# Performance work log

Measured on AMD Instinct MI355X. Metric: run time of the kernel, lower is better.

Reference implementation:

```python
import jax, jax.numpy as jnp
import numpy as np

BINS = 6
THRESH = 0.2
OUT_HW = (240, 240)


def _normalize(x, lo=0.0, hi=1.0):
    # torch: if max-min==0 return zeros, else affine rescale to [lo, hi]
    mn, mx = x.min(), x.max()
    rng = mx - mn
    safe = jnp.where(rng == 0, 1.0, rng)
    out = (x - mn) / safe * (hi - lo) + lo
    return jnp.where(rng == 0, jnp.zeros_like(x), out)


def _ponder(x):
    w = (x.max() - x.mean()) ** 2
    return _normalize(x) * w


def _zero_border(x):
    # zero first/last row and column (works batched over leading dims)
    return (x.at[..., 0, :].set(0.0)
             .at[..., :, 0].set(0.0)
             .at[..., -1, :].set(0.0)
             .at[..., :, -1].set(0.0))


def _rarity(ch):
    # ch: [H, W] single feature channel
    ch = _zero_border(ch)
    ch = _normalize(ch, 0.0, 256.0)
    # torch.histc(bins=BINS, min=0, max=256): last bin includes the max value
    bin_idx = jnp.clip(jnp.floor(ch / (256.0 / BINS)), 0, BINS - 1).astype(jnp.int32)
    hist = jnp.zeros((BINS,), ch.dtype).at[bin_idx].add(1.0)
    hist = -jnp.log(hist / hist.sum() + 0.0001)
    # (channel * bins - 1).long().clamp(0, bins-1): .long() truncates toward zero
    gidx = jnp.clip(jnp.trunc(ch * BINS - 1.0), 0, BINS - 1).astype(jnp.int32)
    dst = _normalize(hist[gidx], 0.0, 1.0)
    return _ponder(dst)


def _apply_rarity(layer):
    # layer: [1, C, H, W] -> per-channel rarity, ponderated sum, threshold
    ch = layer[0]  # [C, H, W]
    r = jax.vmap(_rarity)(ch)  # [C, H, W]
    rz = _zero_border(r)
    # channel 0 keeps its border (torch code only zeroes borders for i >= 1)
    maps = jnp.concatenate([r[:1], rz[1:]], axis=0)
    proc = jax.vmap(_ponder)(maps).sum(0)
    proc = _normalize(proc, 0.0, 1.0)
    return jnp.where(proc < THRESH, 0.0, proc)


def _group(layer):
    resized = jax.image.resize(_apply_rarity(layer), OUT_HW, 'bilinear')
    # pack of one layer: fuse_itti == map_ponderation of the single map
    return _normalize(_ponder(resized), 0.0, 256.0)


def _forward(l1, l2, l3, l4, l5):
    groups = jnp.stack([_group(l) for l in (l1, l2, l3, l4, l5)], axis=-1)  # [240,240,5]
    return groups.sum(-1), groups


def setup_inputs() -> dict:
    key = jax.random.key(0)
    ks = jax.random.split(key, 5)
    shapes = [(1, 64, 480, 480), (1, 128, 240, 240), (1, 256, 120, 120),
              (1, 512, 60, 60), (1, 512, 30, 30)]
    return {f"l{i+1}": jax.random.uniform(ks[i], shapes[i], jnp.float32)
            for i in range(5)}


def reference(l1, l2, l3, l4, l5):
    return _forward(l1, l2, l3, l4, l5)
```

## Files before the change

### kernel.cpp

```cpp
#include <hip/hip_runtime.h>
#include <math.h>

#define TPB 256

constexpr int DIMS_[5]  = {480, 240, 120, 60, 30};
constexpr int CHS_ [5]  = {64, 128, 256, 512, 512};
constexpr int CHB_ [5]  = {0, 64, 192, 448, 960};
constexpr int TOTCH     = 1472;
constexpr int PROCB_[5] = {0, 230400, 288000, 302400, 306000};
constexpr int PROCTOT   = 306900;

constexpr int O_CHMIN = 0;
constexpr int O_CHMAX = 1472;
constexpr int O_HIST  = 2944;
constexpr int O_GCNT  = 11776;
constexpr int O_CLUT  = 20608;
constexpr int O_BSUM  = O_CLUT + 16 * 1472;
constexpr int O_PMIN  = O_BSUM + 5;
constexpr int O_PMAX  = O_PMIN + 5;
constexpr int O_S3MIN = O_PMAX + 5;
constexpr int O_S3MAX = O_S3MIN + 5;
constexpr int O_S3SUM = O_S3MAX + 5;
constexpr int O_PROC  = 44192;
constexpr int O_RESZ  = O_PROC + PROCTOT;

struct P {
  const float* in[5];
  float* ws;
};

__global__ void k_init(float* ws) {
  int i = blockIdx.x * TPB + threadIdx.x;
  if (i >= O_PROC) return;
  unsigned v = 0u;
  if (i < O_CHMAX) v = 0x7F800000u;
  else if (i >= O_PMIN  && i < O_PMAX)  v = 0x7F800000u;
  else if (i >= O_S3MIN && i < O_S3MAX) v = 0x7F800000u;
  ((unsigned*)ws)[i] = v;
}

template <int L>
__device__ void bodyA(int local, const float* __restrict__ in, float* ws) {
  constexpr int D = DIMS_[L], HW = D * D, HW4 = HW / 4;
  constexpr int BPC = (HW4 + 4095) / 4096;
  int ch = local / BPC, chunk = local % BPC;
  int nvec = HW4 - chunk * 4096; if (nvec > 4096) nvec = 4096;
  const float4* pv = (const float4*)(in + (size_t)ch * HW) + (size_t)chunk * 4096;
  int t = threadIdx.x;
  float mn = INFINITY, mx = 0.0f;
  for (int i = 0; i < 16; i++) {
    int vi = i * TPB + t;
    if (vi < nvec) {
      float4 v = pv[vi];
      float vv[4] = {v.x, v.y, v.z, v.w};
      int e0 = (chunk * 4096 + vi) * 4;
      #pragma unroll
      for (int j = 0; j < 4; j++) {
        int e = e0 + j, y = e / D, x = e - y * D;
        bool inr = ((unsigned)(x - 1) < (unsigned)(D - 2)) && ((unsigned)(y - 1) < (unsigned)(D - 2));
        float s = inr ? vv[j] : 0.0f;
        mn = fminf(mn, s); mx = fmaxf(mx, s);
      }
    }
  }
  for (int o = 32; o; o >>= 1) { mn = fminf(mn, __shfl_down(mn, o)); mx = fmaxf(mx, __shfl_down(mx, o)); }
  __shared__ float smn[4], smx[4];
  int w = t >> 6;
  if ((t & 63) == 0) { smn[w] = mn; smx[w] = mx; }
  __syncthreads();
  if (t == 0) {
    mn = fminf(fminf(smn[0], smn[1]), fminf(smn[2], smn[3]));
    mx = fmaxf(fmaxf(smx[0], smx[1]), fmaxf(smx[2], smx[3]));
    int g = CHB_[L] + ch;
    atomicMin((unsigned*)ws + O_CHMIN + g, __float_as_uint(mn));
    atomicMax((unsigned*)ws + O_CHMAX + g, __float_as_uint(mx));
  }
}
__global__ void kA(P p) {
  int b = blockIdx.x;
  if      (b <  960) bodyA<0>(b,        p.in[0], p.ws);
  else if (b < 1472) bodyA<1>(b -  960, p.in[1], p.ws);
  else if (b < 1728) bodyA<2>(b - 1472, p.in[2], p.ws);
  else if (b < 2240) bodyA<3>(b - 1728, p.in[3], p.ws);
  else               bodyA<4>(b - 2240, p.in[4], p.ws);
}

__global__ void kTB(P p) {
  int ch = blockIdx.x;
  float* ws = p.ws;
  int l = (ch < 64) ? 0 : (ch < 192) ? 1 : (ch < 448) ? 2 : (ch < 960) ? 3 : 4;
  int D = DIMS_[l];
  float mn = ws[O_CHMIN + ch], mx = ws[O_CHMAX + ch];
  float rng = mx - mn;
  float th0, th1, th2, th3, th4, tg0, tg1, tg2, tg3, tg4;
  if (rng == 0.0f) {
    th0 = th1 = th2 = th3 = th4 = tg0 = tg1 = tg2 = tg3 = tg4 = INFINITY;
  } else {
    th0 = mn + rng * (1.0f / 6.0f); th1 = mn + rng * (2.0f / 6.0f);
    th2 = mn + rng * (3.0f / 6.0f); th3 = mn + rng * (4.0f / 6.0f);
    th4 = mn + rng * (5.0f / 6.0f);
    tg0 = mn + rng * (2.0f / 1536.0f); tg1 = mn + rng * (3.0f / 1536.0f);
    tg2 = mn + rng * (4.0f / 1536.0f); tg3 = mn + rng * (5.0f / 1536.0f);
    tg4 = mn + rng * (6.0f / 1536.0f);
  }
  int t = threadIdx.x;
  if (t == 0) {
    float* T = ws + O_CLUT + (size_t)ch * 16;
    T[0] = th0; T[1] = th1; T[2] = th2; T[3] = th3; T[4] = th4;
    T[5] = tg0; T[6] = tg1; T[7] = tg2; T[8] = tg3; T[9] = tg4;
  }
  const float* in = p.in[l] + (size_t)(ch - CHB_[l]) * D * D;
  int nb = 4 * D - 4;
  unsigned cH0 = 0, cH1 = 0, cH2 = 0, cH3 = 0, cH4 = 0;
  unsigned cG0 = 0, cG1 = 0, cG2 = 0, cG3 = 0, cG4 = 0, nval = 0;
  for (int j = t; j < nb; j += TPB) {
    int y, x;
    if (j < D)            { y = 0;               x = j;          }
    else if (j < 2 * D)   { y = D - 1;           x = j - D;      }
    else if (j < 3 * D - 2){ y = j - 2 * D + 1;  x = 0;          }
    else                  { y = j - (3 * D - 2) + 1; x = D - 1;  }
    float v = in[y * D + x];
    nval += __popcll(__ballot(1));
    cH0 += __popcll(__ballot(v >= th0)); cH1 += __popcll(__ballot(v >= th1));
    cH2 += __popcll(__ballot(v >= th2)); cH3 += __popcll(__ballot(v >= th3));
    cH4 += __popcll(__ballot(v >= th4));
    cG0 += __popcll(__ballot(v >= tg0)); cG1 += __popcll(__ballot(v >= tg1));
    cG2 += __popcll(__ballot(v >= tg2)); cG3 += __popcll(__ballot(v >= tg3));
    cG4 += __popcll(__ballot(v >= tg4));
  }
  unsigned* H = (unsigned*)ws + O_HIST + ch * 6;
  unsigned* G = (unsigned*)ws + O_GCNT + ch * 6;
  if ((t & 63) == 0) {
    atomicAdd(H + 0, (unsigned)(-(int)(nval - cH0)));
    atomicAdd(H + 1, (unsigned)(-(int)(cH0 - cH1)));
    atomicAdd(H + 2, (unsigned)(-(int)(cH1 - cH2)));
    atomicAdd(H + 3, (unsigned)(-(int)(cH2 - cH3)));
    atomicAdd(H + 4, (unsigned)(-(int)(cH3 - cH4)));
    atomicAdd(H + 5, (unsigned)(-(int)cH4));
    atomicAdd(G + 0, (unsigned)(-(int)(nval - cG0)));
    atomicAdd(G + 1, (unsigned)(-(int)(cG0 - cG1)));
    atomicAdd(G + 2, (unsigned)(-(int)(cG1 - cG2)));
    atomicAdd(G + 3, (unsigned)(-(int)(cG2 - cG3)));
    atomicAdd(G + 4, (unsigned)(-(int)(cG3 - cG4)));
    atomicAdd(G + 5, (unsigned)(-(int)cG4));
  }
  if (t == 0) {
    int hb0 = (0.0f >= th0) + (0.0f >= th1) + (0.0f >= th2) + (0.0f >= th3) + (0.0f >= th4);
    int gb0 = (0.0f >= tg0) + (0.0f >= tg1) + (0.0f >= tg2) + (0.0f >= tg3) + (0.0f >= tg4);
    atomicAdd(H + hb0, (unsigned)nb);
    atomicAdd(G + gb0, (unsigned)nb);
  }
}

template <int L>
__device__ void bodyB(int local, const float* __restrict__ in, float* ws) {
  constexpr int D = DIMS_[L], HW = D * D, HW4 = HW / 4;
  constexpr int BPC = (HW4 + 4095) / 4096;
  int ch = local / BPC, chunk = local % BPC;
  int g = CHB_[L] + ch;
  const float* T = ws + O_CLUT + (size_t)g * 16;
  float th0 = T[0], th1 = T[1], th2 = T[2], th3 = T[3], th4 = T[4];
  float tg0 = T[5], tg1 = T[6], tg2 = T[7], tg3 = T[8], tg4 = T[9];
  int nvec = HW4 - chunk * 4096; if (nvec > 4096) nvec = 4096;
  const float4* pv = (const float4*)(in + (size_t)ch * HW) + (size_t)chunk * 4096;
  int t = threadIdx.x;
  unsigned cH0 = 0, cH1 = 0, cH2 = 0, cH3 = 0, cH4 = 0;
  unsigned cG0 = 0, cG1 = 0, cG2 = 0, cG3 = 0, cG4 = 0, nv4 = 0;
  for (int i = 0; i < 16; i++) {
    int vi = i * TPB + t;
    if (vi < nvec) {
      float4 v = pv[vi];
      nv4 += __popcll(__ballot(1));
      float vv[4] = {v.x, v.y, v.z, v.w};
      #pragma unroll
      for (int j = 0; j < 4; j++) {
        float x = vv[j];
        cH0 += __popcll(__ballot(x >= th0)); cH1 += __popcll(__ballot(x >= th1));
        cH2 += __popcll(__ballot(x >= th2)); cH3 += __popcll(__ballot(x >= th3));
        cH4 += __popcll(__ballot(x >= th4));
        cG0 += __popcll(__ballot(x >= tg0)); cG1 += __popcll(__ballot(x >= tg1));
        cG2 += __popcll(__ballot(x >= tg2)); cG3 += __popcll(__ballot(x >= tg3));
        cG4 += __popcll(__ballot(x >= tg4));
      }
    }
  }
  if ((t & 63) == 0) {
    unsigned tot = nv4 * 4u;
    unsigned* H = (unsigned*)ws + O_HIST + g * 6;
    unsigned* G = (unsigned*)ws + O_GCNT + g * 6;
    atomicAdd(H + 0, tot - cH0); atomicAdd(H + 1, cH0 - cH1);
    atomicAdd(H + 2, cH1 - cH2); atomicAdd(H + 3, cH2 - cH3);
    atomicAdd(H + 4, cH3 - cH4); atomicAdd(H + 5, cH4);
    atomicAdd(G + 0, tot - cG0); atomicAdd(G + 1, cG0 - cG1);
    atomicAdd(G + 2, cG1 - cG2); atomicAdd(G + 3, cG2 - cG3);
    atomicAdd(G + 4, cG3 - cG4); atomicAdd(G + 5, cG4);
  }
}
__global__ void kB(P p) {
  int b = blockIdx.x;
  if      (b <  960) bodyB<0>(b,        p.in[0], p.ws);
  else if (b < 1472) bodyB<1>(b -  960, p.in[1], p.ws);
  else if (b < 1728) bodyB<2>(b - 1472, p.in[2], p.ws);
  else if (b < 2240) bodyB<3>(b - 1728, p.in[3], p.ws);
  else               bodyB<4>(b - 2240, p.in[4], p.ws);
}

__global__ void kS(P p) {
  int ch = blockIdx.x * TPB + threadIdx.x;
  if (ch >= TOTCH) return;
  float* ws = p.ws;
  int l = (ch < 64) ? 0 : (ch < 192) ? 1 : (ch < 448) ? 2 : (ch < 960) ? 3 : 4;
  int D = DIMS_[l];
  int HW = D * D;
  int c0 = ch - CHB_[l];
  unsigned hc[6], gc[6];
  unsigned* H = (unsigned*)ws + O_HIST + ch * 6;
  unsigned* G = (unsigned*)ws + O_GCNT + ch * 6;
  #pragma unroll
  for (int k = 0; k < 6; k++) { hc[k] = H[k]; gc[k] = G[k]; }
  float HWf = (float)HW;
  float nh[6];
  #pragma unroll
  for (int k = 0; k < 6; k++) nh[k] = -logf((float)hc[k] / HWf + 1e-4f);
  float dmn = INFINITY, dmx = -INFINITY;
  #pragma unroll
  for (int k = 0; k < 6; k++) if (gc[k]) { dmn = fminf(dmn, nh[k]); dmx = fmaxf(dmx, nh[k]); }
  float dr = dmx - dmn;
  float dstn[6];
  #pragma unroll
  for (int k = 0; k < 6; k++) dstn[k] = (dr == 0.0f) ? 0.0f : ((nh[k] - dmn) / dr);
  float maxv = (dr == 0.0f) ? 0.0f : 1.0f;
  double s1 = 0.0;
  #pragma unroll
  for (int k = 0; k < 6; k++) s1 += (double)gc[k] * (double)dstn[k];
  float mean1 = (float)(s1 / (double)HW);
  float w1 = maxv - mean1; w1 *= w1;
  float lut1[6];
  #pragma unroll
  for (int k = 0; k < 6; k++) lut1[k] = dstn[k] * w1;
  const float* T = ws + O_CLUT + (size_t)ch * 16;
  int gb = (0.0f >= T[5]) + (0.0f >= T[6]) + (0.0f >= T[7]) + (0.0f >= T[8]) + (0.0f >= T[9]);
  unsigned bcnt = (unsigned)(4 * D - 4);
  float lmn, lmx;
  double s2 = 0.0;
  if (c0 == 0) {
    lmn = INFINITY; lmx = -INFINITY;
    #pragma unroll
    for (int k = 0; k < 6; k++) if (gc[k]) {
      lmn = fminf(lmn, lut1[k]); lmx = fmaxf(lmx, lut1[k]);
      s2 += (double)gc[k] * (double)lut1[k];
    }
  } else {
    lmn = 0.0f; lmx = 0.0f;
    #pragma unroll
    for (int k = 0; k < 6; k++) {
      unsigned ic = gc[k] - ((k == gb) ? bcnt : 0u);
      if (ic) {
        lmn = fminf(lmn, lut1[k]); lmx = fmaxf(lmx, lut1[k]);
        s2 += (double)ic * (double)lut1[k];
      }
    }
  }
  float mean2 = (float)(s2 / (double)HW);
  float w2 = lmx - mean2; w2 *= w2;
  float r2 = lmx - lmn;
  float lout[6];
  #pragma unroll
  for (int k = 0; k < 6; k++) lout[k] = (r2 == 0.0f) ? 0.0f : (((lut1[k] - lmn) / r2) * w2);
  float* LT = ws + O_CLUT + (size_t)ch * 16 + 10;
  #pragma unroll
  for (int k = 0; k < 6; k++) LT[k] = lout[k];
  float bc = (c0 == 0) ? lout[gb] : ((r2 == 0.0f) ? 0.0f : (((0.0f - lmn) / r2) * w2));
  atomicAdd(ws + O_BSUM + l, bc);
}

template <int L>
__device__ void bodyC(int local, const float* __restrict__ in, float* ws,
                      float* slut, float* sred) {
  constexpr int D = DIMS_[L], HW = D * D, HW4 = HW / 4, C = CHS_[L];
  constexpr int Q = C / 4;
  int t = threadIdx.x, lane = t & 63, w = t >> 6;
  const float* gl = ws + O_CLUT + (size_t)CHB_[L] * 16;
  for (int i = t; i < C * 16; i += TPB) slut[i] = gl[i];
  __syncthreads();
  int p4 = local * 64 + lane;
  bool valid = p4 < HW4;
  float a0 = 0.0f, a1 = 0.0f, a2 = 0.0f, a3 = 0.0f;
  if (valid) {
    const float4* bp = (const float4*)in + p4 + (size_t)(w * Q) * HW4;
    const float* su = slut + (size_t)(w * Q) * 16;
    #pragma unroll 4
    for (int c = 0; c < Q; c++) {
      float4 v = bp[(size_t)c * HW4];
      const float* cl = su + c * 16 + 5;
      float g0 = cl[0], g1 = cl[1], g2 = cl[2], g3 = cl[3], g4 = cl[4];
      float l0 = cl[5], l1 = cl[6], l2 = cl[7], l3 = cl[8], l4 = cl[9], l5 = cl[10];
      float s;
      s = (v.x >= g0) ? l1 : l0; s = (v.x >= g1) ? l2 : s; s = (v.x >= g2) ? l3 : s;
      s = (v.x >= g3) ? l4 : s;  s = (v.x >= g4) ? l5 : s; a0 += s;
      s = (v.y >= g0) ? l1 : l0; s = (v.y >= g1) ? l2 : s; s = (v.y >= g2) ? l3 : s;
      s = (v.y >= g3) ? l4 : s;  s = (v.y >= g4) ? l5 : s; a1 += s;
      s = (v.z >= g0) ? l1 : l0; s = (v.z >= g1) ? l2 : s; s = (v.z >= g2) ? l3 : s;
      s = (v.z >= g3) ? l4 : s;  s = (v.z >= g4) ? l5 : s; a2 += s;
      s = (v.w >= g0) ? l1 : l0; s = (v.w >= g1) ? l2 : s; s = (v.w >= g2) ? l3 : s;
      s = (v.w >= g3) ? l4 : s;  s = (v.w >= g4) ? l5 : s; a3 += s;
    }
  }
  sred[0 * 256 + w * 64 + lane] = a0;
  sred[1 * 256 + w * 64 + lane] = a1;
  sred[2 * 256 + w * 64 + lane] = a2;
  sred[3 * 256 + w * 64 + lane] = a3;
  __syncthreads();
  if (w == 0) {
    float o[4];
    #pragma unroll
    for (int j = 0; j < 4; j++)
      o[j] = sred[j * 256 + lane] + sred[j * 256 + 64 + lane] +
             sred[j * 256 + 128 + lane] + sred[j * 256 + 192 + lane];
    float bs = ws[O_BSUM + L];
    int px0 = p4 * 4;
    #pragma unroll
    for (int j = 0; j < 4; j++) {
      int px = px0 + j, y = px / D, x = px - y * D;
      bool inr = ((unsigned)(x - 1) < (unsigned)(D - 2)) && ((unsigned)(y - 1) < (unsigned)(D - 2));
      if (!inr) o[j] = bs;
    }
    float mn, mx;
    if (valid) {
      float4* procL4 = (float4*)(ws + O_PROC + PROCB_[L]);
      procL4[p4] = make_float4(o[0], o[1], o[2], o[3]);
      mn = fminf(fminf(o[0], o[1]), fminf(o[2], o[3]));
      mx = fmaxf(fmaxf(o[0], o[1]), fmaxf(o[2], o[3]));
    } else { mn = INFINITY; mx = 0.0f; }
    for (int s = 32; s; s >>= 1) { mn = fminf(mn, __shfl_down(mn, s)); mx = fmaxf(mx, __shfl_down(mx, s)); }
    if (lane == 0) {
      atomicMin((unsigned*)ws + O_PMIN + L, __float_as_uint(mn));
      atomicMax((unsigned*)ws + O_PMAX + L, __float_as_uint(mx));
    }
  }
}
__global__ __launch_bounds__(TPB) void kC(P p) {
  __shared__ float slut[512 * 16];
  __shared__ float sred[1024];
  int b = blockIdx.x;
  if      (b <  900) bodyC<0>(b,        p.in[0], p.ws, slut, sred);
  else if (b < 1125) bodyC<1>(b -  900, p.in[1], p.ws, slut, sred);
  else if (b < 1182) bodyC<2>(b - 1125, p.in[2], p.ws, slut, sred);
  else if (b < 1197) bodyC<3>(b - 1182, p.in[3], p.ws, slut, sred);
  else               bodyC<4>(b - 1197, p.in[4], p.ws, slut, sred);
}

template <int L>
__device__ float bodyF(int px, float* ws) {
  constexpr int D = DIMS_[L];
  constexpr float INV = (float)D / 240.0f;
  constexpr float KS = (INV > 1.0f) ? INV : 1.0f;
  int oy = px / 240, ox = px - oy * 240;
  float mnv = __uint_as_float(((unsigned*)ws)[O_PMIN + L]);
  float mxv = __uint_as_float(((unsigned*)ws)[O_PMAX + L]);
  float pr = mxv - mnv;
  const float* procL = ws + O_PROC + PROCB_[L];
  float sfy = ((float)oy + 0.5f) * INV - 0.5f;
  float sfx = ((float)ox + 0.5f) * INV - 0.5f;
  int y0 = (int)ceilf(sfy - KS);  if (y0 < 0) y0 = 0;
  int y1 = (int)floorf(sfy + KS); if (y1 > D - 1) y1 = D - 1;
  int x0 = (int)ceilf(sfx - KS);  if (x0 < 0) x0 = 0;
  int x1 = (int)floorf(sfx + KS); if (x1 > D - 1) x1 = D - 1;
  float wsx = 0.0f;
  for (int jx = x0; jx <= x1; jx++) wsx += fmaxf(1.0f - fabsf(sfx - (float)jx) / KS, 0.0f);
  float acc = 0.0f, wsy = 0.0f;
  for (int jy = y0; jy <= y1; jy++) {
    float wy = fmaxf(1.0f - fabsf(sfy - (float)jy) / KS, 0.0f);
    wsy += wy;
    if (wy > 0.0f) {
      const float* row = procL + jy * D;
      float rs = 0.0f;
      for (int jx = x0; jx <= x1; jx++) {
        float wx = fmaxf(1.0f - fabsf(sfx - (float)jx) / KS, 0.0f);
        if (wx > 0.0f) {
          float v = row[jx];
          float tv = (pr == 0.0f) ? 0.0f : ((v - mnv) / pr);
          tv = (tv < 0.2f) ? 0.0f : tv;
          rs += wx * tv;
        }
      }
      acc += wy * rs;
    }
  }
  return acc / (wsy * wsx);
}
__global__ void kF(P p) {
  float* ws = p.ws;
  int b = blockIdx.x, l = b / 225;
  int px = (b - l * 225) * TPB + threadIdx.x;
  float res;
  switch (l) {
    case 0: res = bodyF<0>(px, ws); break;
    case 1: res = bodyF<1>(px, ws); break;
    case 2: res = bodyF<2>(px, ws); break;
    case 3: res = bodyF<3>(px, ws); break;
    default: res = bodyF<4>(px, ws); break;
  }
  ws[O_RESZ + l * 57600 + px] = res;
  float mn = res, mx = res, s = res;
  for (int o = 32; o; o >>= 1) {
    mn = fminf(mn, __shfl_down(mn, o));
    mx = fmaxf(mx, __shfl_down(mx, o));
    s += __shfl_down(s, o);
  }
  __shared__ float smn[4], smx[4], ssm[4];
  int t = threadIdx.x, w = t >> 6;
  if ((t & 63) == 0) { smn[w] = mn; smx[w] = mx; ssm[w] = s; }
  __syncthreads();
  if (t == 0) {
    mn = fminf(fminf(smn[0], smn[1]), fminf(smn[2], smn[3]));
    mx = fmaxf(fmaxf(smx[0], smx[1]), fmaxf(smx[2], smx[3]));
    s = ssm[0] + ssm[1] + ssm[2] + ssm[3];
    atomicMin((unsigned*)ws + O_S3MIN + l, __float_as_uint(mn));
    atomicMax((unsigned*)ws + O_S3MAX + l, __float_as_uint(mx));
    atomicAdd(ws + O_S3SUM + l, s);
  }
}

__global__ void kG2(P p, float* __restrict__ out) {
  float* ws = p.ws;
  int px = blockIdx.x * TPB + threadIdx.x;
  float sum = 0.0f;
  #pragma unroll
  for (int l = 0; l < 5; l++) {
    float v = ws[O_RESZ + l * 57600 + px];
    float mn3 = __uint_as_float(((unsigned*)ws)[O_S3MIN + l]);
    float mx3 = __uint_as_float(((unsigned*)ws)[O_S3MAX + l]);
    float mean3 = ws[O_S3SUM + l] / 57600.0f;
    float r3 = mx3 - mn3;
    float ov;
    if (r3 == 0.0f) ov = 0.0f;
    else {
      float w3 = mx3 - mean3; w3 *= w3;
      if (w3 == 0.0f) ov = 0.0f;
      else ov = ((v - mn3) / r3) * w3 / w3 * 256.0f;
    }
    out[57600 + px * 5 + l] = ov;
    sum += ov;
  }
  out[px] = sum;
}

extern "C" void kernel_launch(void* const* d_in, const int* in_sizes, int n_in,
                              void* d_out, int out_size, void* d_ws, size_t ws_size,
                              hipStream_t stream) {
  (void)in_sizes; (void)n_in; (void)out_size; (void)ws_size;
  P p;
  for (int i = 0; i < 5; i++) p.in[i] = (const float*)d_in[i];
  p.ws = (float*)d_ws;
  float* out = (float*)d_out;

  k_init<<<(O_PROC + TPB - 1) / TPB, TPB, 0, stream>>>(p.ws);
  kA  <<<2752, TPB, 0, stream>>>(p);
  kTB <<<1472, TPB, 0, stream>>>(p);
  kB  <<<2752, TPB, 0, stream>>>(p);
  kS  <<<6,    TPB, 0, stream>>>(p);
  kC  <<<1201, TPB, 0, stream>>>(p);
  kF  <<<1125, TPB, 0, stream>>>(p);
  kG2 <<<225,  TPB, 0, stream>>>(p, out);
}
```

Baseline: 339.3 us.

## Split channel loop in kC across 64-channel chunks, drop border kernel

Result: faster. 294.0 us (-13.4%).

```diff
diff --git a/kernel.cpp b/kernel.cpp
--- a/kernel.cpp
+++ b/kernel.cpp
@@ -23,15 +23,29 @@
 constexpr int O_S3SUM = O_S3MAX + 5;
 constexpr int O_PROC  = 44192;
 constexpr int O_RESZ  = O_PROC + PROCTOT;
+constexpr int N_INIT  = O_PROC + PROCTOT;
 
 struct P {
   const float* in[5];
   float* ws;
 };
 
+__device__ __forceinline__ void mk_hthr(float mn, float rng, float* th) {
+  if (rng == 0.0f) { th[0]=th[1]=th[2]=th[3]=th[4]=INFINITY; return; }
+  th[0] = mn + rng * (1.0f / 6.0f); th[1] = mn + rng * (2.0f / 6.0f);
+  th[2] = mn + rng * (3.0f / 6.0f); th[3] = mn + rng * (4.0f / 6.0f);
+  th[4] = mn + rng * (5.0f / 6.0f);
+}
+__device__ __forceinline__ void mk_gthr(float mn, float rng, float* tg) {
+  if (rng == 0.0f) { tg[0]=tg[1]=tg[2]=tg[3]=tg[4]=INFINITY; return; }
+  tg[0] = mn + rng * (2.0f / 1536.0f); tg[1] = mn + rng * (3.0f / 1536.0f);
+  tg[2] = mn + rng * (4.0f / 1536.0f); tg[3] = mn + rng * (5.0f / 1536.0f);
+  tg[4] = mn + rng * (6.0f / 1536.0f);
+}
+
 __global__ void k_init(float* ws) {
   int i = blockIdx.x * TPB + threadIdx.x;
-  if (i >= O_PROC) return;
+  if (i >= N_INIT) return;
   unsigned v = 0u;
   if (i < O_CHMAX) v = 0x7F800000u;
   else if (i >= O_PMIN  && i < O_PMAX)  v = 0x7F800000u;
@@ -85,82 +99,17 @@
   else               bodyA<4>(b - 2240, p.in[4], p.ws);
 }
 
-__global__ void kTB(P p) {
-  int ch = blockIdx.x;
-  float* ws = p.ws;
-  int l = (ch < 64) ? 0 : (ch < 192) ? 1 : (ch < 448) ? 2 : (ch < 960) ? 3 : 4;
-  int D = DIMS_[l];
-  float mn = ws[O_CHMIN + ch], mx = ws[O_CHMAX + ch];
-  float rng = mx - mn;
-  float th0, th1, th2, th3, th4, tg0, tg1, tg2, tg3, tg4;
-  if (rng == 0.0f) {
-    th0 = th1 = th2 = th3 = th4 = tg0 = tg1 = tg2 = tg3 = tg4 = INFINITY;
-  } else {
-    th0 = mn + rng * (1.0f / 6.0f); th1 = mn + rng * (2.0f / 6.0f);
-    th2 = mn + rng * (3.0f / 6.0f); th3 = mn + rng * (4.0f / 6.0f);
-    th4 = mn + rng * (5.0f / 6.0f);
-    tg0 = mn + rng * (2.0f / 1536.0f); tg1 = mn + rng * (3.0f / 1536.0f);
-    tg2 = mn + rng * (4.0f / 1536.0f); tg3 = mn + rng * (5.0f / 1536.0f);
-    tg4 = mn + rng * (6.0f / 1536.0f);
-  }
-  int t = threadIdx.x;
-  if (t == 0) {
-    float* T = ws + O_CLUT + (size_t)ch * 16;
-    T[0] = th0; T[1] = th1; T[2] = th2; T[3] = th3; T[4] = th4;
-    T[5] = tg0; T[6] = tg1; T[7] = tg2; T[8] = tg3; T[9] = tg4;
-  }
-  const float* in = p.in[l] + (size_t)(ch - CHB_[l]) * D * D;
-  int nb = 4 * D - 4;
-  unsigned cH0 = 0, cH1 = 0, cH2 = 0, cH3 = 0, cH4 = 0;
-  unsigned cG0 = 0, cG1 = 0, cG2 = 0, cG3 = 0, cG4 = 0, nval = 0;
-  for (int j = t; j < nb; j += TPB) {
-    int y, x;
-    if (j < D)            { y = 0;               x = j;          }
-    else if (j < 2 * D)   { y = D - 1;           x = j - D;      }
-    else if (j < 3 * D - 2){ y = j - 2 * D + 1;  x = 0;          }
-    else                  { y = j - (3 * D - 2) + 1; x = D - 1;  }
-    float v = in[y * D + x];
-    nval += __popcll(__ballot(1));
-    cH0 += __popcll(__ballot(v >= th0)); cH1 += __popcll(__ballot(v >= th1));
-    cH2 += __popcll(__ballot(v >= th2)); cH3 += __popcll(__ballot(v >= th3));
-    cH4 += __popcll(__ballot(v >= th4));
-    cG0 += __popcll(__ballot(v >= tg0)); cG1 += __popcll(__ballot(v >= tg1));
-    cG2 += __popcll(__ballot(v >= tg2)); cG3 += __popcll(__ballot(v >= tg3));
-    cG4 += __popcll(__ballot(v >= tg4));
-  }
-  unsigned* H = (unsigned*)ws + O_HIST + ch * 6;
-  unsigned* G = (unsigned*)ws + O_GCNT + ch * 6;
-  if ((t & 63) == 0) {
-    atomicAdd(H + 0, (unsigned)(-(int)(nval - cH0)));
-    atomicAdd(H + 1, (unsigned)(-(int)(cH0 - cH1)));
-    atomicAdd(H + 2, (unsigned)(-(int)(cH1 - cH2)));
-    atomicAdd(H + 3, (unsigned)(-(int)(cH2 - cH3)));
-    atomicAdd(H + 4, (unsigned)(-(int)(cH3 - cH4)));
-    atomicAdd(H + 5, (unsigned)(-(int)cH4));
-    atomicAdd(G + 0, (unsigned)(-(int)(nval - cG0)));
-    atomicAdd(G + 1, (unsigned)(-(int)(cG0 - cG1)));
-    atomicAdd(G + 2, (unsigned)(-(int)(cG1 - cG2)));
-    atomicAdd(G + 3, (unsigned)(-(int)(cG2 - cG3)));
-    atomicAdd(G + 4, (unsigned)(-(int)(cG3 - cG4)));
-    atomicAdd(G + 5, (unsigned)(-(int)cG4));
-  }
-  if (t == 0) {
-    int hb0 = (0.0f >= th0) + (0.0f >= th1) + (0.0f >= th2) + (0.0f >= th3) + (0.0f >= th4);
-    int gb0 = (0.0f >= tg0) + (0.0f >= tg1) + (0.0f >= tg2) + (0.0f >= tg3) + (0.0f >= tg4);
-    atomicAdd(H + hb0, (unsigned)nb);
-    atomicAdd(G + gb0, (unsigned)nb);
-  }
-}
-
 template <int L>
 __device__ void bodyB(int local, const float* __restrict__ in, float* ws) {
   constexpr int D = DIMS_[L], HW = D * D, HW4 = HW / 4;
   constexpr int BPC = (HW4 + 4095) / 4096;
+  constexpr int DQ = D / 4;
   int ch = local / BPC, chunk = local % BPC;
   int g = CHB_[L] + ch;
-  const float* T = ws + O_CLUT + (size_t)g * 16;
-  float th0 = T[0], th1 = T[1], th2 = T[2], th3 = T[3], th4 = T[4];
-  float tg0 = T[5], tg1 = T[6], tg2 = T[7], tg3 = T[8], tg4 = T[9];
+  float mn = ws[O_CHMIN + g], mx = ws[O_CHMAX + g], rng = mx - mn;
+  float th[5], tg[5];
+  mk_hthr(mn, rng, th);
+  mk_gthr(mn, rng, tg);
   int nvec = HW4 - chunk * 4096; if (nvec > 4096) nvec = 4096;
   const float4* pv = (const float4*)(in + (size_t)ch * HW) + (size_t)chunk * 4096;
   int t = threadIdx.x;
@@ -170,17 +119,34 @@
     int vi = i * TPB + t;
     if (vi < nvec) {
       float4 v = pv[vi];
+      float vv[4] = {v.x, v.y, v.z, v.w};
+      int f4i = chunk * 4096 + vi;
+      if constexpr (D % 4 == 0) {
+        int y = f4i / DQ, xq = f4i - y * DQ;
+        if (y == 0 || y == D - 1) { vv[0] = vv[1] = vv[2] = vv[3] = 0.0f; }
+        else {
+          if (xq == 0)      vv[0] = 0.0f;
+          if (xq == DQ - 1) vv[3] = 0.0f;
+        }
+      } else {
+        int e0 = f4i * 4;
+        #pragma unroll
+        for (int j = 0; j < 4; j++) {
+          int e = e0 + j, y = e / D, x = e - y * D;
+          bool inr = ((unsigned)(x - 1) < (unsigned)(D - 2)) && ((unsigned)(y - 1) < (unsigned)(D - 2));
+          if (!inr) vv[j] = 0.0f;
+        }
+      }
       nv4 += __popcll(__ballot(1));
-      float vv[4] = {v.x, v.y, v.z, v.w};
       #pragma unroll
       for (int j = 0; j < 4; j++) {
         float x = vv[j];
-        cH0 += __popcll(__ballot(x >= th0)); cH1 += __popcll(__ballot(x >= th1));
-        cH2 += __popcll(__ballot(x >= th2)); cH3 += __popcll(__ballot(x >= th3));
-        cH4 += __popcll(__ballot(x >= th4));
-        cG0 += __popcll(__ballot(x >= tg0)); cG1 += __popcll(__ballot(x >= tg1));
-        cG2 += __popcll(__ballot(x >= tg2)); cG3 += __popcll(__ballot(x >= tg3));
-        cG4 += __popcll(__ballot(x >= tg4));
+        cH0 += __popcll(__ballot(x >= th[0])); cH1 += __popcll(__ballot(x >= th[1]));
+        cH2 += __popcll(__ballot(x >= th[2])); cH3 += __popcll(__ballot(x >= th[3]));
+        cH4 += __popcll(__ballot(x >= th[4]));
+        cG0 += __popcll(__ballot(x >= tg[0])); cG1 += __popcll(__ballot(x >= tg[1]));
+        cG2 += __popcll(__ballot(x >= tg[2])); cG3 += __popcll(__ballot(x >= tg[3]));
+        cG4 += __popcll(__ballot(x >= tg[4]));
       }
     }
   }
@@ -238,8 +204,10 @@
   float lut1[6];
   #pragma unroll
   for (int k = 0; k < 6; k++) lut1[k] = dstn[k] * w1;
-  const float* T = ws + O_CLUT + (size_t)ch * 16;
-  int gb = (0.0f >= T[5]) + (0.0f >= T[6]) + (0.0f >= T[7]) + (0.0f >= T[8]) + (0.0f >= T[9]);
+  float mnc = ws[O_CHMIN + ch], mxc = ws[O_CHMAX + ch];
+  float tg[5];
+  mk_gthr(mnc, mxc - mnc, tg);
+  int gb = (0.0f >= tg[0]) + (0.0f >= tg[1]) + (0.0f >= tg[2]) + (0.0f >= tg[3]) + (0.0f >= tg[4]);
   unsigned bcnt = (unsigned)(4 * D - 4);
   float lmn, lmx;
   double s2 = 0.0;
@@ -267,9 +235,11 @@
   float lout[6];
   #pragma unroll
   for (int k = 0; k < 6; k++) lout[k] = (r2 == 0.0f) ? 0.0f : (((lut1[k] - lmn) / r2) * w2);
-  float* LT = ws + O_CLUT + (size_t)ch * 16 + 10;
-  #pragma unroll
-  for (int k = 0; k < 6; k++) LT[k] = lout[k];
+  float* T = ws + O_CLUT + (size_t)ch * 16;
+  #pragma unroll
+  for (int k = 0; k < 5; k++) T[5 + k] = tg[k];
+  #pragma unroll
+  for (int k = 0; k < 6; k++) T[10 + k] = lout[k];
   float bc = (c0 == 0) ? lout[gb] : ((r2 == 0.0f) ? 0.0f : (((0.0f - lmn) / r2) * w2));
   atomicAdd(ws + O_BSUM + l, bc);
 }
@@ -278,19 +248,22 @@
 __device__ void bodyC(int local, const float* __restrict__ in, float* ws,
                       float* slut, float* sred) {
   constexpr int D = DIMS_[L], HW = D * D, HW4 = HW / 4, C = CHS_[L];
-  constexpr int Q = C / 4;
+  constexpr int NT  = (HW4 + 63) / 64;
+  constexpr int NCH = C / 64;
+  int tile = local % NT, chunk = local / NT;
+  int cbase = CHB_[L] + chunk * 64;
   int t = threadIdx.x, lane = t & 63, w = t >> 6;
-  const float* gl = ws + O_CLUT + (size_t)CHB_[L] * 16;
-  for (int i = t; i < C * 16; i += TPB) slut[i] = gl[i];
+  const float* gl = ws + O_CLUT + (size_t)cbase * 16;
+  for (int i = t; i < 1024; i += TPB) slut[i] = gl[i];
   __syncthreads();
-  int p4 = local * 64 + lane;
+  int p4 = tile * 64 + lane;
   bool valid = p4 < HW4;
   float a0 = 0.0f, a1 = 0.0f, a2 = 0.0f, a3 = 0.0f;
   if (valid) {
-    const float4* bp = (const float4*)in + p4 + (size_t)(w * Q) * HW4;
-    const float* su = slut + (size_t)(w * Q) * 16;
+    const float4* bp = (const float4*)in + (size_t)(chunk * 64 + w * 16) * HW4 + p4;
+    const float* su = slut + (w * 16) * 16;
     #pragma unroll 4
-    for (int c = 0; c < Q; c++) {
+    for (int c = 0; c < 16; c++) {
       float4 v = bp[(size_t)c * HW4];
       const float* cl = su + c * 16 + 5;
       float g0 = cl[0], g1 = cl[1], g2 = cl[2], g3 = cl[3], g4 = cl[4];
@@ -311,43 +284,75 @@
   sred[2 * 256 + w * 64 + lane] = a2;
   sred[3 * 256 + w * 64 + lane] = a3;
   __syncthreads();
-  if (w == 0) {
+  if (w == 0 && valid) {
     float o[4];
     #pragma unroll
     for (int j = 0; j < 4; j++)
       o[j] = sred[j * 256 + lane] + sred[j * 256 + 64 + lane] +
              sred[j * 256 + 128 + lane] + sred[j * 256 + 192 + lane];
     float bs = ws[O_BSUM + L];
+    float* procL = ws + O_PROC + PROCB_[L];
     int px0 = p4 * 4;
-    #pragma unroll
-    for (int j = 0; j < 4; j++) {
-      int px = px0 + j, y = px / D, x = px - y * D;
-      bool inr = ((unsigned)(x - 1) < (unsigned)(D - 2)) && ((unsigned)(y - 1) < (unsigned)(D - 2));
-      if (!inr) o[j] = bs;
-    }
-    float mn, mx;
-    if (valid) {
-      float4* procL4 = (float4*)(ws + O_PROC + PROCB_[L]);
-      procL4[p4] = make_float4(o[0], o[1], o[2], o[3]);
-      mn = fminf(fminf(o[0], o[1]), fminf(o[2], o[3]));
-      mx = fmaxf(fmaxf(o[0], o[1]), fmaxf(o[2], o[3]));
-    } else { mn = INFINITY; mx = 0.0f; }
-    for (int s = 32; s; s >>= 1) { mn = fminf(mn, __shfl_down(mn, s)); mx = fmaxf(mx, __shfl_down(mx, s)); }
-    if (lane == 0) {
-      atomicMin((unsigned*)ws + O_PMIN + L, __float_as_uint(mn));
-      atomicMax((unsigned*)ws + O_PMAX + L, __float_as_uint(mx));
+    if constexpr (NCH == 1) {
+      #pragma unroll
+      for (int j = 0; j < 4; j++) {
+        int px = px0 + j, y = px / D, x = px - y * D;
+        bool inr = ((unsigned)(x - 1) < (unsigned)(D - 2)) && ((unsigned)(y - 1) < (unsigned)(D - 2));
+        if (!inr) o[j] = bs;
+      }
+      ((float4*)procL)[p4] = make_float4(o[0], o[1], o[2], o[3]);
+    } else {
+      #pragma unroll
+      for (int j = 0; j < 4; j++) {
+        int px = px0 + j, y = px / D, x = px - y * D;
+        bool inr = ((unsigned)(x - 1) < (unsigned)(D - 2)) && ((unsigned)(y - 1) < (unsigned)(D - 2));
+        if (inr) atomicAdd(procL + px, o[j]);
+        else if (chunk == 0) procL[px] = bs;
+      }
     }
   }
 }
 __global__ __launch_bounds__(TPB) void kC(P p) {
-  __shared__ float slut[512 * 16];
+  __shared__ float slut[1024];
   __shared__ float sred[1024];
   int b = blockIdx.x;
   if      (b <  900) bodyC<0>(b,        p.in[0], p.ws, slut, sred);
-  else if (b < 1125) bodyC<1>(b -  900, p.in[1], p.ws, slut, sred);
-  else if (b < 1182) bodyC<2>(b - 1125, p.in[2], p.ws, slut, sred);
-  else if (b < 1197) bodyC<3>(b - 1182, p.in[3], p.ws, slut, sred);
-  else               bodyC<4>(b - 1197, p.in[4], p.ws, slut, sred);
+  else if (b < 1350) bodyC<1>(b -  900, p.in[1], p.ws, slut, sred);
+  else if (b < 1578) bodyC<2>(b - 1350, p.in[2], p.ws, slut, sred);
+  else if (b < 1698) bodyC<3>(b - 1578, p.in[3], p.ws, slut, sred);
+  else               bodyC<4>(b - 1698, p.in[4], p.ws, slut, sred);
+}
+
+template <int L>
+__device__ void bodyD(int chunk, float* ws) {
+  constexpr int HW = DIMS_[L] * DIMS_[L];
+  const float* pr = ws + O_PROC + PROCB_[L];
+  int t = threadIdx.x;
+  float mn = INFINITY, mx = 0.0f;
+  #pragma unroll
+  for (int i = 0; i < 16; i++) {
+    int idx = chunk * 4096 + i * TPB + t;
+    if (idx < HW) { float v = pr[idx]; mn = fminf(mn, v); mx = fmaxf(mx, v); }
+  }
+  for (int o = 32; o; o >>= 1) { mn = fminf(mn, __shfl_down(mn, o)); mx = fmaxf(mx, __shfl_down(mx, o)); }
+  __shared__ float smn[4], smx[4];
+  int w = t >> 6;
+  if ((t & 63) == 0) { smn[w] = mn; smx[w] = mx; }
+  __syncthreads();
+  if (t == 0) {
+    mn = fminf(fminf(smn[0], smn[1]), fminf(smn[2], smn[3]));
+    mx = fmaxf(fmaxf(smx[0], smx[1]), fmaxf(smx[2], smx[3]));
+    atomicMin((unsigned*)ws + O_PMIN + L, __float_as_uint(mn));
+    atomicMax((unsigned*)ws + O_PMAX + L, __float_as_uint(mx));
+  }
+}
+__global__ void kD(P p) {
+  int b = blockIdx.x;
+  if      (b < 57) bodyD<0>(b,      p.ws);
+  else if (b < 72) bodyD<1>(b - 57, p.ws);
+  else if (b < 76) bodyD<2>(b - 72, p.ws);
+  else if (b < 77) bodyD<3>(b - 76, p.ws);
+  else             bodyD<4>(b - 77, p.ws);
 }
 
 template <int L>
@@ -455,12 +460,12 @@
   p.ws = (float*)d_ws;
   float* out = (float*)d_out;
 
-  k_init<<<(O_PROC + TPB - 1) / TPB, TPB, 0, stream>>>(p.ws);
+  k_init<<<(N_INIT + TPB - 1) / TPB, TPB, 0, stream>>>(p.ws);
   kA  <<<2752, TPB, 0, stream>>>(p);
-  kTB <<<1472, TPB, 0, stream>>>(p);
   kB  <<<2752, TPB, 0, stream>>>(p);
   kS  <<<6,    TPB, 0, stream>>>(p);
-  kC  <<<1201, TPB, 0, stream>>>(p);
+  kC  <<<1730, TPB, 0, stream>>>(p);
+  kD  <<<78,   TPB, 0, stream>>>(p);
   kF  <<<1125, TPB, 0, stream>>>(p);
   kG2 <<<225,  TPB, 0, stream>>>(p, out);
 }
```
